# Kernel optimization log

Measured on AMD Instinct MI355X. Metric: run time of the kernel, lower is better.

Reference implementation:

```python
import jax, jax.numpy as jnp
import numpy as np

B, N = 256, 65536          # batch, num_tokens (world.num_tokens == N)
VOCAB = 50257
ALPHA = 0.5                # dirichlet concentration
EPS = 1e-7                 # gumbel eps


def setup_inputs() -> dict:
    key = jax.random.key(0)
    kb, kt, ku, kd = jax.random.split(key, 4)
    batch = jax.random.randint(kb, (B, N), 0, VOCAB, dtype=jnp.int32)
    t = jax.random.uniform(kt, (B,), dtype=jnp.float32)
    U = jax.random.uniform(ku, (B, N), dtype=jnp.float32)
    # dirichlet(alpha=0.5) sample over the token axis, one simplex per row
    D = jax.random.dirichlet(kd, ALPHA * jnp.ones((N,), jnp.float32), shape=(B,)).astype(jnp.float32)
    return {"batch": batch, "t": t, "U": U, "D": D}


def cosine_schedule(t):
    return 1.0 - jnp.cos(jnp.pi * t / 2)


def cosine_weight(t, eps=1e-3):
    t_adj = t * (1 - 2 * eps) + eps
    return 0.5 * jnp.pi * jnp.sin(jnp.pi * t_adj / 2)


def binary_topk(weights, ks):
    # weights: [B, N] float; ks: [B, 1] int -> bool mask marking the top-k per row
    Bn, Nn = weights.shape
    idx = jnp.argsort(-weights, axis=-1)                     # descending order indices
    rank = jnp.broadcast_to(jnp.arange(Nn), (Bn, Nn))        # rank of each sorted slot
    mask = jnp.zeros((Bn, Nn), dtype=bool)
    mask = mask.at[jnp.arange(Bn)[:, None], idx].set(ks > rank)
    return mask


def reference(batch, t, U, D):
    r = cosine_schedule(t)                                   # mask rate per sample [B]
    w = cosine_weight(t)                                     # loss weight per sample [B]
    G = -jnp.log(-jnp.log(U + EPS) + EPS)                    # gumbel noise [B, N]
    weights = G + jnp.log(D)                                 # gumbel + log-dirichlet
    ks = (N * r).astype(jnp.int32)[:, None]                  # [B, 1] tokens to mask
    mask = binary_topk(weights, ks)                          # [B, N] bool
    return mask, w
```

## Files before the change

kernel.cpp:

```cpp
#include <hip/hip_runtime.h>
#include <math.h>

#define BB 256
#define NN 65536
#define NT 1024
#define CAP 2048
#define MARGIN 2e-3f

__device__ __forceinline__ unsigned int f2sort(float f) {
    unsigned int b = __float_as_uint(f);
    return (b & 0x80000000u) ? ~b : (b | 0x80000000u);
}
__device__ __forceinline__ float sort2f(unsigned int u) {
    unsigned int b = (u & 0x80000000u) ? (u & 0x7fffffffu) : ~u;
    return __uint_as_float(b);
}

__device__ __forceinline__ unsigned int wexact(float u, float d) {
    float t1 = u + 1e-7f;
    float t2 = (float)log((double)t1);
    float t3 = (-t2) + 1e-7f;
    float G  = -(float)log((double)t3);
    float lgD = (float)log((double)d);
    return f2sort(G + lgD);
}

__device__ __forceinline__ unsigned int wfast(float u, float d) {
    float t1 = u + 1e-7f;
    float t3 = -__logf(t1) + 1e-7f;
    float G  = -__logf(t3);
    return f2sort(G + __logf(d));
}

__device__ __forceinline__ bool finite_f(float f) {
    return (__float_as_uint(f) & 0x7f800000u) != 0x7f800000u;
}

#define CHUNKS(OP) OP(0) OP(1) OP(2) OP(3) OP(4) OP(5) OP(6) OP(7) \
                   OP(8) OP(9) OP(10) OP(11) OP(12) OP(13) OP(14) OP(15)

#define PASS1SEL(KKV) \
    { const int b0 = tid * 8; unsigned int cs = 0; \
      _Pragma("unroll") for (int i = 0; i < 8; i++) cs += hist[b0 + i]; \
      chunkSum[tid] = cs; } \
    __syncthreads(); \
    if (tid < 64) { \
        const int c0i = lane * 16; unsigned int s = 0; \
        _Pragma("unroll") for (int i = 0; i < 16; i++) s += chunkSum[c0i + i]; \
        unsigned int suf = s; \
        _Pragma("unroll") for (int off = 1; off < 64; off <<= 1) { \
            unsigned int tv = __shfl_down(suf, off); if (lane + off < 64) suf += tv; } \
        unsigned int above = suf - s; \
        if (suf >= (KKV) && above < (KKV)) { \
            unsigned int cum = above; \
            for (int ci = c0i + 15; ci >= c0i; ci--) { \
                unsigned int cch = chunkSum[ci]; \
                if (cum + cch >= (KKV)) { \
                    for (int b = ci * 8 + 7; ; b--) { \
                        unsigned int c2 = hist[b]; \
                        if (cum + c2 >= (KKV)) { s_sel = (unsigned int)b; s_kneed = (KKV) - cum; s_eq = c2; break; } \
                        cum += c2; } \
                    break; } \
                cum += cch; } } } \
    __syncthreads();

#define PASS2SEL(P, KN) \
    if (tid < 64) { \
        const int c0i = lane * 16; unsigned int s = 0; \
        _Pragma("unroll") for (int i = 0; i < 16; i++) s += hist[c0i + i]; \
        unsigned int suf = s; \
        _Pragma("unroll") for (int off = 1; off < 64; off <<= 1) { \
            unsigned int tv = __shfl_down(suf, off); if (lane + off < 64) suf += tv; } \
        unsigned int above = suf - s; \
        if (suf >= (KN) && above < (KN)) { \
            unsigned int cum = above; \
            for (int b = c0i + 15; ; b--) { \
                unsigned int c2 = hist[b]; \
                if (cum + c2 >= (KN)) { s_sel = ((P) << 10) | (unsigned int)b; s_kneed = (KN) - cum; s_eq = c2; break; } \
                cum += c2; } } } \
    __syncthreads();

#define PASS3SEL(P, KN) \
    if (tid < 64) { \
        const int c0i = lane * 8; unsigned int s = 0; \
        _Pragma("unroll") for (int i = 0; i < 8; i++) s += hist[c0i + i]; \
        unsigned int suf = s; \
        _Pragma("unroll") for (int off = 1; off < 64; off <<= 1) { \
            unsigned int tv = __shfl_down(suf, off); if (lane + off < 64) suf += tv; } \
        unsigned int above = suf - s; \
        if (suf >= (KN) && above < (KN)) { \
            unsigned int cum = above; \
            for (int b = c0i + 7; ; b--) { \
                unsigned int c2 = hist[b]; \
                if (cum + c2 >= (KN)) { s_sel = ((P) << 9) | (unsigned int)b; s_kneed = (KN) - cum; s_eq = c2; break; } \
                cum += c2; } } } \
    __syncthreads();

__global__ __launch_bounds__(NT) __attribute__((amdgpu_waves_per_eu(4, 4)))
void md_fused_kernel(const float* __restrict__ Tt,
                     const float* __restrict__ U,
                     const float* __restrict__ D,
                     float* __restrict__ out,
                     float* __restrict__ wout) {
    const int row = blockIdx.x;
    const int tid = threadIdx.x;
    const int lane = tid & 63;

    const float* Ur = U + (size_t)row * NN;
    const float* Dr = D + (size_t)row * NN;
    float* Or = out + (size_t)row * NN;

    __shared__ unsigned int hist[8192];
    __shared__ unsigned int chunkSum[NT];
    __shared__ unsigned int bandU[CAP];
    __shared__ int bandIdx[CAP];
    __shared__ unsigned int bitmap[2048];
    __shared__ int s_tielist[1024];
    __shared__ unsigned int s_sel, s_kneed, s_eq;
    __shared__ int s_A, s_bandCnt, s_tiecnt, s_tieidx;

    const float t = Tt[row];
    const float pf = (float)M_PI;
    float aa = pf * t;
    float bbv = aa * 0.5f;
    float c0 = (float)cos((double)bbv);
    float r  = 1.0f - c0;
    const int k = (int)(65536.0f * r);
    if (tid == 0) {
        float tadj = t * 0.998f + 0.001f;
        float arg  = (pf * tadj) * 0.5f;
        wout[row] = (float)(0.5 * M_PI) * (float)sin((double)arg);
    }

    if (k <= 0 || k >= NN) {
        const float fill = (k >= NN) ? 1.0f : 0.0f;
        float4 f4 = make_float4(fill, fill, fill, fill);
        for (int j = 0; j < 16; j++)
            *(float4*)(Or + j * 4096 + tid * 4) = f4;
        return;
    }
    const unsigned int kk = (unsigned int)k;

    uint4 v0, v1, v2, v3, v4, v5, v6, v7, v8, v9, v10, v11, v12, v13, v14, v15;

    for (int i = tid; i < 8192; i += NT) hist[i] = 0;
    if (tid == 0) { s_A = 0; s_bandCnt = 0; }
    __syncthreads();

#define COMPF(J) { \
        int e = (J) * 4096 + tid * 4; \
        float4 u4 = *(const float4*)(Ur + e); \
        float4 d4 = *(const float4*)(Dr + e); \
        v##J.x = wfast(u4.x, d4.x); \
        v##J.y = wfast(u4.y, d4.y); \
        v##J.z = wfast(u4.z, d4.z); \
        v##J.w = wfast(u4.w, d4.w); \
        atomicAdd(&hist[v##J.x >> 19], 1u); \
        atomicAdd(&hist[v##J.y >> 19], 1u); \
        atomicAdd(&hist[v##J.z >> 19], 1u); \
        atomicAdd(&hist[v##J.w >> 19], 1u); }
    CHUNKS(COMPF)
#undef COMPF
    __syncthreads();

    PASS1SEL(kk)
    const unsigned int p13 = s_sel;
    const unsigned int kn1 = s_kneed;
    hist[tid] = 0;
    __syncthreads();
#define P2F(J) { \
        if ((v##J.x >> 19) == p13) atomicAdd(&hist[(v##J.x >> 9) & 1023u], 1u); \
        if ((v##J.y >> 19) == p13) atomicAdd(&hist[(v##J.y >> 9) & 1023u], 1u); \
        if ((v##J.z >> 19) == p13) atomicAdd(&hist[(v##J.z >> 9) & 1023u], 1u); \
        if ((v##J.w >> 19) == p13) atomicAdd(&hist[(v##J.w >> 9) & 1023u], 1u); }
    CHUNKS(P2F)
#undef P2F
    __syncthreads();
    PASS2SEL(p13, kn1)

    const unsigned int p23 = s_sel;
    const float loF = sort2f(p23 << 9) - MARGIN;
    const float hiF = sort2f((p23 << 9) | 511u) + MARGIN;
    const bool badBand = !(finite_f(loF) && finite_f(hiF));
    const unsigned int lo_u = f2sort(loF);
    const unsigned int hi_u = f2sort(hiF);

    bitmap[tid] = 0;
    bitmap[tid + 1024] = 0;
    {
        int cnt = 0;
#define ACNT1(X) cnt += (int)((X) > hi_u);
#define ACNT(J) ACNT1(v##J.x) ACNT1(v##J.y) ACNT1(v##J.z) ACNT1(v##J.w)
        CHUNKS(ACNT)
#undef ACNT
#undef ACNT1
#pragma unroll
        for (int off = 32; off >= 1; off >>= 1) cnt += __shfl_down(cnt, off);
        if (lane == 0) atomicAdd(&s_A, cnt);
    }
#define GATH1(J, C, CI) { unsigned int uu = v##J.C; \
        if (uu >= lo_u && uu <= hi_u) { \
            int slot = atomicAdd(&s_bandCnt, 1); \
            if (slot < CAP) bandIdx[slot] = (J) * 4096 + tid * 4 + (CI); } }
#define GATH(J) GATH1(J, x, 0) GATH1(J, y, 1) GATH1(J, z, 2) GATH1(J, w, 3)
    CHUNKS(GATH)
#undef GATH
#undef GATH1
    __syncthreads();

    const int bandCnt = s_bandCnt;
    const int kb = k - s_A;
    const bool fallback = badBand || (bandCnt > CAP) || (kb < 0) || (kb > bandCnt);

    if (!fallback) {
        for (int j = tid; j < bandCnt; j += NT) {
            int idx = bandIdx[j];
            bandU[j] = wexact(Ur[idx], Dr[idx]);
        }
        __syncthreads();
        for (int j = tid; j < bandCnt; j += NT) {
            unsigned int me = bandU[j];
            int mi = bandIdx[j];
            int rk = 0;
            for (int i = 0; i < bandCnt; i++) {
                unsigned int o = bandU[i];
                rk += (int)((o > me) || (o == me && bandIdx[i] < mi));
            }
            if (rk < kb) atomicOr(&bitmap[mi >> 5], 1u << (mi & 31));
        }
        __syncthreads();
        const int b0 = (tid & 7) * 4;
#define WRF(J) { \
        int e = (J) * 4096 + tid * 4; \
        unsigned int wb = bitmap[(J) * 128 + (tid >> 3)]; \
        float4 m; \
        m.x = ((v##J.x > hi_u) || ((wb >> (b0 + 0)) & 1u)) ? 1.0f : 0.0f; \
        m.y = ((v##J.y > hi_u) || ((wb >> (b0 + 1)) & 1u)) ? 1.0f : 0.0f; \
        m.z = ((v##J.z > hi_u) || ((wb >> (b0 + 2)) & 1u)) ? 1.0f : 0.0f; \
        m.w = ((v##J.w > hi_u) || ((wb >> (b0 + 3)) & 1u)) ? 1.0f : 0.0f; \
        *(float4*)(Or + e) = m; }
        CHUNKS(WRF)
#undef WRF
        return;
    }

    __syncthreads();
    for (int i = tid; i < 8192; i += NT) hist[i] = 0;
    __syncthreads();
#define COMPE(J) { \
        int e = (J) * 4096 + tid * 4; \
        float4 u4 = *(const float4*)(Ur + e); \
        float4 d4 = *(const float4*)(Dr + e); \
        v##J.x = wexact(u4.x, d4.x); \
        v##J.y = wexact(u4.y, d4.y); \
        v##J.z = wexact(u4.z, d4.z); \
        v##J.w = wexact(u4.w, d4.w); \
        atomicAdd(&hist[v##J.x >> 19], 1u); \
        atomicAdd(&hist[v##J.y >> 19], 1u); \
        atomicAdd(&hist[v##J.z >> 19], 1u); \
        atomicAdd(&hist[v##J.w >> 19], 1u); }
    CHUNKS(COMPE)
#undef COMPE
    __syncthreads();

    PASS1SEL(kk)
    const unsigned int q13 = s_sel;
    const unsigned int en1 = s_kneed;
    hist[tid] = 0;
    __syncthreads();
#define P2E(J) { \
        if ((v##J.x >> 19) == q13) atomicAdd(&hist[(v##J.x >> 9) & 1023u], 1u); \
        if ((v##J.y >> 19) == q13) atomicAdd(&hist[(v##J.y >> 9) & 1023u], 1u); \
        if ((v##J.z >> 19) == q13) atomicAdd(&hist[(v##J.z >> 9) & 1023u], 1u); \
        if ((v##J.w >> 19) == q13) atomicAdd(&hist[(v##J.w >> 9) & 1023u], 1u); }
    CHUNKS(P2E)
#undef P2E
    __syncthreads();
    PASS2SEL(q13, en1)

    const unsigned int q23 = s_sel;
    const unsigned int en2 = s_kneed;
    if (tid < 512) hist[tid] = 0;
    __syncthreads();
#define P3E(J) { \
        if ((v##J.x >> 9) == q23) atomicAdd(&hist[v##J.x & 511u], 1u); \
        if ((v##J.y >> 9) == q23) atomicAdd(&hist[v##J.y & 511u], 1u); \
        if ((v##J.z >> 9) == q23) atomicAdd(&hist[v##J.z & 511u], 1u); \
        if ((v##J.w >> 9) == q23) atomicAdd(&hist[v##J.w & 511u], 1u); }
    CHUNKS(P3E)
#undef P3E
    __syncthreads();
    PASS3SEL(q23, en2)

    const unsigned int theta = s_sel;
    const unsigned int kneedF = s_kneed, eqF = s_eq;
    const bool needOrder = (kneedF < eqF);
    int istar = NN;
    if (needOrder) {
        if (tid == 0) s_tiecnt = 0;
        __syncthreads();
#define TIE1(J, C, CI) if (v##J.C == theta) { \
            int pos = atomicAdd(&s_tiecnt, 1); \
            if (pos < 1024) s_tielist[pos] = (J) * 4096 + tid * 4 + (CI); }
#define TIE(J) TIE1(J, x, 0) TIE1(J, y, 1) TIE1(J, z, 2) TIE1(J, w, 3)
        CHUNKS(TIE)
#undef TIE
#undef TIE1
        __syncthreads();
        if (tid == 0) {
            int E = s_tiecnt; if (E > 1024) E = 1024;
            for (int aI = 1; aI < E; aI++) {
                int val = s_tielist[aI]; int bI = aI - 1;
                while (bI >= 0 && s_tielist[bI] > val) { s_tielist[bI + 1] = s_tielist[bI]; bI--; }
                s_tielist[bI + 1] = val;
            }
            int kk2 = (int)kneedF; if (kk2 > E) kk2 = E; if (kk2 < 1) kk2 = 1;
            s_tieidx = s_tielist[kk2 - 1];
        }
        __syncthreads();
        istar = s_tieidx;
    }

#define MVE(u, idx) ((((u) > theta) || ((u) == theta && (!needOrder || (idx) <= istar))) ? 1.0f : 0.0f)
#define WRE(J) { \
        int e = (J) * 4096 + tid * 4; \
        float4 m; \
        m.x = MVE(v##J.x, e + 0); \
        m.y = MVE(v##J.y, e + 1); \
        m.z = MVE(v##J.z, e + 2); \
        m.w = MVE(v##J.w, e + 3); \
        *(float4*)(Or + e) = m; }
    CHUNKS(WRE)
#undef WRE
#undef MVE
}

extern "C" void kernel_launch(void* const* d_in, const int* in_sizes, int n_in,
                              void* d_out, int out_size, void* d_ws, size_t ws_size,
                              hipStream_t stream) {
    const float* T = (const float*)d_in[1];
    const float* U = (const float*)d_in[2];
    const float* D = (const float*)d_in[3];
    float* out = (float*)d_out;
    float* wout = out + (size_t)BB * NN;

    md_fused_kernel<<<BB, NT, 0, stream>>>(T, U, D, out, wout);
}
```

Measured before the change: 237.7 us.

## Keep 16-bit keys in LDS instead of 64 registers and coarsen radix digits

The kernel no longer holds all 64 sort keys per thread in registers. It stores the top 16 bits of each key in a 128KB LDS buffer and runs an 11+5-bit two-pass select on those 16-bit keys. That frees registers, which is why the waves-per-eu attribute is dropped. The band check and final mask now use the 16-bit prefixes, so the candidate band is wider. The rare exact fallback path recomputes keys from global memory on every pass instead of caching them. In exchange the main path pays extra LDS traffic for each pass, and the large shared allocation limits the kernel to one block per CU.

```diff
diff --git a/kernel.cpp b/kernel.cpp
--- a/kernel.cpp
+++ b/kernel.cpp
@@ -35,9 +35,6 @@
 __device__ __forceinline__ bool finite_f(float f) {
     return (__float_as_uint(f) & 0x7f800000u) != 0x7f800000u;
 }
-
-#define CHUNKS(OP) OP(0) OP(1) OP(2) OP(3) OP(4) OP(5) OP(6) OP(7) \
-                   OP(8) OP(9) OP(10) OP(11) OP(12) OP(13) OP(14) OP(15)
 
 #define PASS1SEL(KKV) \
     { const int b0 = tid * 8; unsigned int cs = 0; \
@@ -96,7 +93,7 @@
                 cum += c2; } } } \
     __syncthreads();
 
-__global__ __launch_bounds__(NT) __attribute__((amdgpu_waves_per_eu(4, 4)))
+__global__ __launch_bounds__(NT)
 void md_fused_kernel(const float* __restrict__ Tt,
                      const float* __restrict__ U,
                      const float* __restrict__ D,
@@ -110,14 +107,18 @@
     const float* Dr = D + (size_t)row * NN;
     float* Or = out + (size_t)row * NN;
 
-    __shared__ unsigned int hist[8192];
-    __shared__ unsigned int chunkSum[NT];
-    __shared__ unsigned int bandU[CAP];
-    __shared__ int bandIdx[CAP];
-    __shared__ unsigned int bitmap[2048];
-    __shared__ int s_tielist[1024];
+    __shared__ __align__(16) unsigned char smem[159744];
+    unsigned short* sval = (unsigned short*)smem;
+    unsigned int* h11   = (unsigned int*)(smem + 131072);
+    unsigned int* bitmap = (unsigned int*)(smem + 131072);
+    unsigned int* csum  = (unsigned int*)(smem + 139264);
+    int* bandIdx        = (int*)(smem + 143360);
+    unsigned int* bandU = (unsigned int*)(smem + 151552);
+
+    __shared__ unsigned int s_b1, s_kneed1, s_b2;
+    __shared__ int s_A, s_bandCnt;
     __shared__ unsigned int s_sel, s_kneed, s_eq;
-    __shared__ int s_A, s_bandCnt, s_tiecnt, s_tieidx;
+    __shared__ int s_tiecnt, s_tieidx;
 
     const float t = Tt[row];
     const float pf = (float)M_PI;
@@ -141,78 +142,125 @@
     }
     const unsigned int kk = (unsigned int)k;
 
-    uint4 v0, v1, v2, v3, v4, v5, v6, v7, v8, v9, v10, v11, v12, v13, v14, v15;
-
-    for (int i = tid; i < 8192; i += NT) hist[i] = 0;
+    for (int i = tid; i < 2048; i += NT) h11[i] = 0;
     if (tid == 0) { s_A = 0; s_bandCnt = 0; }
     __syncthreads();
 
-#define COMPF(J) { \
-        int e = (J) * 4096 + tid * 4; \
-        float4 u4 = *(const float4*)(Ur + e); \
-        float4 d4 = *(const float4*)(Dr + e); \
-        v##J.x = wfast(u4.x, d4.x); \
-        v##J.y = wfast(u4.y, d4.y); \
-        v##J.z = wfast(u4.z, d4.z); \
-        v##J.w = wfast(u4.w, d4.w); \
-        atomicAdd(&hist[v##J.x >> 19], 1u); \
-        atomicAdd(&hist[v##J.y >> 19], 1u); \
-        atomicAdd(&hist[v##J.z >> 19], 1u); \
-        atomicAdd(&hist[v##J.w >> 19], 1u); }
-    CHUNKS(COMPF)
-#undef COMPF
-    __syncthreads();
-
-    PASS1SEL(kk)
-    const unsigned int p13 = s_sel;
-    const unsigned int kn1 = s_kneed;
-    hist[tid] = 0;
-    __syncthreads();
-#define P2F(J) { \
-        if ((v##J.x >> 19) == p13) atomicAdd(&hist[(v##J.x >> 9) & 1023u], 1u); \
-        if ((v##J.y >> 19) == p13) atomicAdd(&hist[(v##J.y >> 9) & 1023u], 1u); \
-        if ((v##J.z >> 19) == p13) atomicAdd(&hist[(v##J.z >> 9) & 1023u], 1u); \
-        if ((v##J.w >> 19) == p13) atomicAdd(&hist[(v##J.w >> 9) & 1023u], 1u); }
-    CHUNKS(P2F)
-#undef P2F
-    __syncthreads();
-    PASS2SEL(p13, kn1)
-
-    const unsigned int p23 = s_sel;
-    const float loF = sort2f(p23 << 9) - MARGIN;
-    const float hiF = sort2f((p23 << 9) | 511u) + MARGIN;
+    for (int j = 0; j < 16; j++) {
+        int e = j * 4096 + tid * 4;
+        float4 u4 = *(const float4*)(Ur + e);
+        float4 d4 = *(const float4*)(Dr + e);
+        unsigned int w0 = wfast(u4.x, d4.x);
+        unsigned int w1 = wfast(u4.y, d4.y);
+        unsigned int w2 = wfast(u4.z, d4.z);
+        unsigned int w3 = wfast(u4.w, d4.w);
+        uint2 pk;
+        pk.x = (w0 >> 16) | (w1 & 0xFFFF0000u);
+        pk.y = (w2 >> 16) | (w3 & 0xFFFF0000u);
+        *(uint2*)(sval + e) = pk;
+        atomicAdd(&h11[w0 >> 21], 1u);
+        atomicAdd(&h11[w1 >> 21], 1u);
+        atomicAdd(&h11[w2 >> 21], 1u);
+        atomicAdd(&h11[w3 >> 21], 1u);
+    }
+    __syncthreads();
+
+    {
+        unsigned int cs = h11[2 * tid] + h11[2 * tid + 1];
+        csum[tid] = cs;
+    }
+    __syncthreads();
+    if (tid < 64) {
+        const int c0i = lane * 16;
+        unsigned int s = 0;
+#pragma unroll
+        for (int i = 0; i < 16; i++) s += csum[c0i + i];
+        unsigned int suf = s;
+#pragma unroll
+        for (int off = 1; off < 64; off <<= 1) {
+            unsigned int tv = __shfl_down(suf, off);
+            if (lane + off < 64) suf += tv;
+        }
+        unsigned int above = suf - s;
+        if (suf >= kk && above < kk) {
+            unsigned int cum = above;
+            for (int ci = c0i + 15; ci >= c0i; ci--) {
+                unsigned int cch = csum[ci];
+                if (cum + cch >= kk) {
+                    for (int b = 2 * ci + 1; ; b--) {
+                        unsigned int c2 = h11[b];
+                        if (cum + c2 >= kk) { s_b1 = (unsigned int)b; s_kneed1 = kk - cum; break; }
+                        cum += c2;
+                    }
+                    break;
+                }
+                cum += cch;
+            }
+        }
+    }
+    __syncthreads();
+
+    const unsigned int b1 = s_b1;
+    const unsigned int kn1 = s_kneed1;
+    __syncthreads();
+    if (tid < 32) h11[tid] = 0;
+    __syncthreads();
+    for (int j = 0; j < 16; j++) {
+        int e = j * 4096 + tid * 4;
+        uint2 pk = *(const uint2*)(sval + e);
+        unsigned int s0 = pk.x & 0xFFFFu, s1 = pk.x >> 16;
+        unsigned int s2 = pk.y & 0xFFFFu, s3 = pk.y >> 16;
+        if ((s0 >> 5) == b1) atomicAdd(&h11[s0 & 31u], 1u);
+        if ((s1 >> 5) == b1) atomicAdd(&h11[s1 & 31u], 1u);
+        if ((s2 >> 5) == b1) atomicAdd(&h11[s2 & 31u], 1u);
+        if ((s3 >> 5) == b1) atomicAdd(&h11[s3 & 31u], 1u);
+    }
+    __syncthreads();
+    if (tid < 64) {
+        unsigned int c = (lane < 32) ? h11[lane] : 0u;
+        unsigned int suf = c;
+#pragma unroll
+        for (int off = 1; off < 64; off <<= 1) {
+            unsigned int tv = __shfl_down(suf, off);
+            if (lane + off < 64) suf += tv;
+        }
+        if (suf >= kn1 && (suf - c) < kn1) s_b2 = (unsigned int)lane;
+    }
+    __syncthreads();
+
+    const unsigned int T16 = (b1 << 5) | s_b2;
+    const float loF = sort2f(T16 << 16) - MARGIN;
+    const float hiF = sort2f((T16 << 16) | 0xFFFFu) + MARGIN;
     const bool badBand = !(finite_f(loF) && finite_f(hiF));
-    const unsigned int lo_u = f2sort(loF);
-    const unsigned int hi_u = f2sort(hiF);
-
-    bitmap[tid] = 0;
-    bitmap[tid + 1024] = 0;
+    const unsigned int lo16 = f2sort(loF) >> 16;
+    const unsigned int hi16 = f2sort(hiF) >> 16;
+
     {
         int cnt = 0;
-#define ACNT1(X) cnt += (int)((X) > hi_u);
-#define ACNT(J) ACNT1(v##J.x) ACNT1(v##J.y) ACNT1(v##J.z) ACNT1(v##J.w)
-        CHUNKS(ACNT)
-#undef ACNT
-#undef ACNT1
+        for (int j = 0; j < 16; j++) {
+            int e = j * 4096 + tid * 4;
+            uint2 pk = *(const uint2*)(sval + e);
+            unsigned int s0 = pk.x & 0xFFFFu, s1 = pk.x >> 16;
+            unsigned int s2 = pk.y & 0xFFFFu, s3 = pk.y >> 16;
+            cnt += (int)(s0 > hi16) + (int)(s1 > hi16) + (int)(s2 > hi16) + (int)(s3 > hi16);
+            if (s0 >= lo16 && s0 <= hi16) { int sl = atomicAdd(&s_bandCnt, 1); if (sl < CAP) bandIdx[sl] = e + 0; }
+            if (s1 >= lo16 && s1 <= hi16) { int sl = atomicAdd(&s_bandCnt, 1); if (sl < CAP) bandIdx[sl] = e + 1; }
+            if (s2 >= lo16 && s2 <= hi16) { int sl = atomicAdd(&s_bandCnt, 1); if (sl < CAP) bandIdx[sl] = e + 2; }
+            if (s3 >= lo16 && s3 <= hi16) { int sl = atomicAdd(&s_bandCnt, 1); if (sl < CAP) bandIdx[sl] = e + 3; }
+        }
 #pragma unroll
         for (int off = 32; off >= 1; off >>= 1) cnt += __shfl_down(cnt, off);
         if (lane == 0) atomicAdd(&s_A, cnt);
-    }
-#define GATH1(J, C, CI) { unsigned int uu = v##J.C; \
-        if (uu >= lo_u && uu <= hi_u) { \
-            int slot = atomicAdd(&s_bandCnt, 1); \
-            if (slot < CAP) bandIdx[slot] = (J) * 4096 + tid * 4 + (CI); } }
-#define GATH(J) GATH1(J, x, 0) GATH1(J, y, 1) GATH1(J, z, 2) GATH1(J, w, 3)
-    CHUNKS(GATH)
-#undef GATH
-#undef GATH1
+        bitmap[tid] = 0;
+        bitmap[tid + 1024] = 0;
+    }
     __syncthreads();
 
     const int bandCnt = s_bandCnt;
     const int kb = k - s_A;
-    const bool fallback = badBand || (bandCnt > CAP) || (kb < 0) || (kb > bandCnt);
-
-    if (!fallback) {
+    const bool fb = badBand || (bandCnt > CAP) || (kb < 0) || (kb > bandCnt);
+
+    if (!fb) {
         for (int j = tid; j < bandCnt; j += NT) {
             int idx = bandIdx[j];
             bandU[j] = wexact(Ur[idx], Dr[idx]);
@@ -229,110 +277,128 @@
             if (rk < kb) atomicOr(&bitmap[mi >> 5], 1u << (mi & 31));
         }
         __syncthreads();
-        const int b0 = (tid & 7) * 4;
-#define WRF(J) { \
-        int e = (J) * 4096 + tid * 4; \
-        unsigned int wb = bitmap[(J) * 128 + (tid >> 3)]; \
-        float4 m; \
-        m.x = ((v##J.x > hi_u) || ((wb >> (b0 + 0)) & 1u)) ? 1.0f : 0.0f; \
-        m.y = ((v##J.y > hi_u) || ((wb >> (b0 + 1)) & 1u)) ? 1.0f : 0.0f; \
-        m.z = ((v##J.z > hi_u) || ((wb >> (b0 + 2)) & 1u)) ? 1.0f : 0.0f; \
-        m.w = ((v##J.w > hi_u) || ((wb >> (b0 + 3)) & 1u)) ? 1.0f : 0.0f; \
-        *(float4*)(Or + e) = m; }
-        CHUNKS(WRF)
-#undef WRF
+        const int bsh = (tid & 7) * 4;
+        for (int j = 0; j < 16; j++) {
+            int e = j * 4096 + tid * 4;
+            uint2 pk = *(const uint2*)(sval + e);
+            unsigned int wb = bitmap[j * 128 + (tid >> 3)];
+            unsigned int s0 = pk.x & 0xFFFFu, s1 = pk.x >> 16;
+            unsigned int s2 = pk.y & 0xFFFFu, s3 = pk.y >> 16;
+            float4 m;
+            m.x = ((s0 > hi16) || ((wb >> (bsh + 0)) & 1u)) ? 1.0f : 0.0f;
+            m.y = ((s1 > hi16) || ((wb >> (bsh + 1)) & 1u)) ? 1.0f : 0.0f;
+            m.z = ((s2 > hi16) || ((wb >> (bsh + 2)) & 1u)) ? 1.0f : 0.0f;
+            m.w = ((s3 > hi16) || ((wb >> (bsh + 3)) & 1u)) ? 1.0f : 0.0f;
+            *(float4*)(Or + e) = m;
+        }
         return;
     }
 
-    __syncthreads();
-    for (int i = tid; i < 8192; i += NT) hist[i] = 0;
-    __syncthreads();
-#define COMPE(J) { \
-        int e = (J) * 4096 + tid * 4; \
-        float4 u4 = *(const float4*)(Ur + e); \
-        float4 d4 = *(const float4*)(Dr + e); \
-        v##J.x = wexact(u4.x, d4.x); \
-        v##J.y = wexact(u4.y, d4.y); \
-        v##J.z = wexact(u4.z, d4.z); \
-        v##J.w = wexact(u4.w, d4.w); \
-        atomicAdd(&hist[v##J.x >> 19], 1u); \
-        atomicAdd(&hist[v##J.y >> 19], 1u); \
-        atomicAdd(&hist[v##J.z >> 19], 1u); \
-        atomicAdd(&hist[v##J.w >> 19], 1u); }
-    CHUNKS(COMPE)
-#undef COMPE
-    __syncthreads();
-
-    PASS1SEL(kk)
-    const unsigned int q13 = s_sel;
-    const unsigned int en1 = s_kneed;
-    hist[tid] = 0;
-    __syncthreads();
-#define P2E(J) { \
-        if ((v##J.x >> 19) == q13) atomicAdd(&hist[(v##J.x >> 9) & 1023u], 1u); \
-        if ((v##J.y >> 19) == q13) atomicAdd(&hist[(v##J.y >> 9) & 1023u], 1u); \
-        if ((v##J.z >> 19) == q13) atomicAdd(&hist[(v##J.z >> 9) & 1023u], 1u); \
-        if ((v##J.w >> 19) == q13) atomicAdd(&hist[(v##J.w >> 9) & 1023u], 1u); }
-    CHUNKS(P2E)
-#undef P2E
-    __syncthreads();
-    PASS2SEL(q13, en1)
-
-    const unsigned int q23 = s_sel;
-    const unsigned int en2 = s_kneed;
-    if (tid < 512) hist[tid] = 0;
-    __syncthreads();
-#define P3E(J) { \
-        if ((v##J.x >> 9) == q23) atomicAdd(&hist[v##J.x & 511u], 1u); \
-        if ((v##J.y >> 9) == q23) atomicAdd(&hist[v##J.y & 511u], 1u); \
-        if ((v##J.z >> 9) == q23) atomicAdd(&hist[v##J.z & 511u], 1u); \
-        if ((v##J.w >> 9) == q23) atomicAdd(&hist[v##J.w & 511u], 1u); }
-    CHUNKS(P3E)
-#undef P3E
-    __syncthreads();
-    PASS3SEL(q23, en2)
-
-    const unsigned int theta = s_sel;
-    const unsigned int kneedF = s_kneed, eqF = s_eq;
-    const bool needOrder = (kneedF < eqF);
-    int istar = NN;
-    if (needOrder) {
-        if (tid == 0) s_tiecnt = 0;
-        __syncthreads();
-#define TIE1(J, C, CI) if (v##J.C == theta) { \
-            int pos = atomicAdd(&s_tiecnt, 1); \
-            if (pos < 1024) s_tielist[pos] = (J) * 4096 + tid * 4 + (CI); }
-#define TIE(J) TIE1(J, x, 0) TIE1(J, y, 1) TIE1(J, z, 2) TIE1(J, w, 3)
-        CHUNKS(TIE)
-#undef TIE
-#undef TIE1
-        __syncthreads();
-        if (tid == 0) {
-            int E = s_tiecnt; if (E > 1024) E = 1024;
-            for (int aI = 1; aI < E; aI++) {
-                int val = s_tielist[aI]; int bI = aI - 1;
-                while (bI >= 0 && s_tielist[bI] > val) { s_tielist[bI + 1] = s_tielist[bI]; bI--; }
-                s_tielist[bI + 1] = val;
+    {
+        unsigned int* hist = (unsigned int*)smem;
+        unsigned int* chunkSum = (unsigned int*)(smem + 32768);
+        int* s_tielist = (int*)(smem + 143360);
+
+        __syncthreads();
+        for (int i = tid; i < 8192; i += NT) hist[i] = 0;
+        __syncthreads();
+        for (int j = 0; j < 16; j++) {
+            int e = j * 4096 + tid * 4;
+            float4 u4 = *(const float4*)(Ur + e);
+            float4 d4 = *(const float4*)(Dr + e);
+            atomicAdd(&hist[wexact(u4.x, d4.x) >> 19], 1u);
+            atomicAdd(&hist[wexact(u4.y, d4.y) >> 19], 1u);
+            atomicAdd(&hist[wexact(u4.z, d4.z) >> 19], 1u);
+            atomicAdd(&hist[wexact(u4.w, d4.w) >> 19], 1u);
+        }
+        __syncthreads();
+
+        PASS1SEL(kk)
+        const unsigned int q13 = s_sel;
+        const unsigned int en1 = s_kneed;
+        for (int i = tid; i < 1024; i += NT) hist[i] = 0;
+        __syncthreads();
+        for (int j = 0; j < 16; j++) {
+            int e = j * 4096 + tid * 4;
+            float4 u4 = *(const float4*)(Ur + e);
+            float4 d4 = *(const float4*)(Dr + e);
+            unsigned int w0 = wexact(u4.x, d4.x), w1 = wexact(u4.y, d4.y);
+            unsigned int w2 = wexact(u4.z, d4.z), w3 = wexact(u4.w, d4.w);
+            if ((w0 >> 19) == q13) atomicAdd(&hist[(w0 >> 9) & 1023u], 1u);
+            if ((w1 >> 19) == q13) atomicAdd(&hist[(w1 >> 9) & 1023u], 1u);
+            if ((w2 >> 19) == q13) atomicAdd(&hist[(w2 >> 9) & 1023u], 1u);
+            if ((w3 >> 19) == q13) atomicAdd(&hist[(w3 >> 9) & 1023u], 1u);
+        }
+        __syncthreads();
+        PASS2SEL(q13, en1)
+
+        const unsigned int q23 = s_sel;
+        const unsigned int en2 = s_kneed;
+        if (tid < 512) hist[tid] = 0;
+        __syncthreads();
+        for (int j = 0; j < 16; j++) {
+            int e = j * 4096 + tid * 4;
+            float4 u4 = *(const float4*)(Ur + e);
+            float4 d4 = *(const float4*)(Dr + e);
+            unsigned int w0 = wexact(u4.x, d4.x), w1 = wexact(u4.y, d4.y);
+            unsigned int w2 = wexact(u4.z, d4.z), w3 = wexact(u4.w, d4.w);
+            if ((w0 >> 9) == q23) atomicAdd(&hist[w0 & 511u], 1u);
+            if ((w1 >> 9) == q23) atomicAdd(&hist[w1 & 511u], 1u);
+            if ((w2 >> 9) == q23) atomicAdd(&hist[w2 & 511u], 1u);
+            if ((w3 >> 9) == q23) atomicAdd(&hist[w3 & 511u], 1u);
+        }
+        __syncthreads();
+        PASS3SEL(q23, en2)
+
+        const unsigned int theta = s_sel;
+        const unsigned int kneedF = s_kneed, eqF = s_eq;
+        const bool needOrder = (kneedF < eqF);
+        int istar = NN;
+        if (needOrder) {
+            if (tid == 0) s_tiecnt = 0;
+            __syncthreads();
+            for (int j = 0; j < 16; j++) {
+                int e = j * 4096 + tid * 4;
+                float4 u4 = *(const float4*)(Ur + e);
+                float4 d4 = *(const float4*)(Dr + e);
+                unsigned int w[4] = {wexact(u4.x, d4.x), wexact(u4.y, d4.y),
+                                     wexact(u4.z, d4.z), wexact(u4.w, d4.w)};
+                for (int c = 0; c < 4; c++)
+                    if (w[c] == theta) {
+                        int pos = atomicAdd(&s_tiecnt, 1);
+                        if (pos < 1024) s_tielist[pos] = e + c;
+                    }
             }
-            int kk2 = (int)kneedF; if (kk2 > E) kk2 = E; if (kk2 < 1) kk2 = 1;
-            s_tieidx = s_tielist[kk2 - 1];
-        }
-        __syncthreads();
-        istar = s_tieidx;
-    }
-
-#define MVE(u, idx) ((((u) > theta) || ((u) == theta && (!needOrder || (idx) <= istar))) ? 1.0f : 0.0f)
-#define WRE(J) { \
-        int e = (J) * 4096 + tid * 4; \
-        float4 m; \
-        m.x = MVE(v##J.x, e + 0); \
-        m.y = MVE(v##J.y, e + 1); \
-        m.z = MVE(v##J.z, e + 2); \
-        m.w = MVE(v##J.w, e + 3); \
-        *(float4*)(Or + e) = m; }
-    CHUNKS(WRE)
-#undef WRE
-#undef MVE
+            __syncthreads();
+            if (tid == 0) {
+                int E = s_tiecnt; if (E > 1024) E = 1024;
+                for (int aI = 1; aI < E; aI++) {
+                    int val = s_tielist[aI]; int bI = aI - 1;
+                    while (bI >= 0 && s_tielist[bI] > val) { s_tielist[bI + 1] = s_tielist[bI]; bI--; }
+                    s_tielist[bI + 1] = val;
+                }
+                int kk2 = (int)kneedF; if (kk2 > E) kk2 = E; if (kk2 < 1) kk2 = 1;
+                s_tieidx = s_tielist[kk2 - 1];
+            }
+            __syncthreads();
+            istar = s_tieidx;
+        }
+
+        for (int j = 0; j < 16; j++) {
+            int e = j * 4096 + tid * 4;
+            float4 u4 = *(const float4*)(Ur + e);
+            float4 d4 = *(const float4*)(Dr + e);
+            unsigned int w[4] = {wexact(u4.x, d4.x), wexact(u4.y, d4.y),
+                                 wexact(u4.z, d4.z), wexact(u4.w, d4.w)};
+            float4 m;
+            float* mp = &m.x;
+            for (int c = 0; c < 4; c++) {
+                bool in = (w[c] > theta) || (w[c] == theta && (!needOrder || (e + c) <= istar));
+                mp[c] = in ? 1.0f : 0.0f;
+            }
+            *(float4*)(Or + e) = m;
+        }
+    }
 }
 
 extern "C" void kernel_launch(void* const* d_in, const int* in_sizes, int n_in,
```

Result: slower. 704.3 us (+196.3%).
